# Kernel optimization log

Measured on AMD Instinct MI355X. Metric: run time of the kernel, lower is better.

Reference implementation:

```python
import jax, jax.numpy as jnp
import numpy as np

LEAKY_SLOPE = 0.01  # torch nn.LeakyReLU default


def leaky_relu(x):
    return jnp.where(x >= 0, x, LEAKY_SLOPE * x)


def rgcn_conv(x, edge_index, edge_type, w_rel, w_root, b_conv):
    # PyG RGCNConv: out = x @ W_root + b + sum_r mean_{edges of rel r into i}(x_src @ W_r)
    n = x.shape[0]
    src, dst = edge_index[0], edge_index[1]
    out = x @ w_root + b_conv
    num_rel = w_rel.shape[0]
    for r in range(num_rel):  # small fixed relation count
        mask = (edge_type == r)
        msg = x[src] @ w_rel[r]                      # [E, H]
        msg = jnp.where(mask[:, None], msg, 0.0)
        agg = jax.ops.segment_sum(msg, dst, num_segments=n)          # [N, H]
        cnt = jax.ops.segment_sum(mask.astype(x.dtype), dst, num_segments=n)
        out = out + agg / jnp.maximum(cnt, 1.0)[:, None]             # mean aggr
    return out


def setup_inputs() -> dict:
    key = jax.random.key(0)
    ks = jax.random.split(key, 10)
    N, E, D_IN, H, OUT, R = 50000, 600000, 768, 128, 3, 2
    s_in = 1.0 / np.sqrt(D_IN)
    s_h = 1.0 / np.sqrt(H)
    return {
        "feature": jax.random.normal(ks[0], (N, D_IN), dtype=jnp.float32),
        "edge_index": jax.random.randint(ks[1], (2, E), 0, N, dtype=jnp.int64),
        "edge_type": jax.random.randint(ks[2], (E,), 0, R, dtype=jnp.int64),
        "w_in": jax.random.uniform(ks[3], (D_IN, H), jnp.float32, -s_in, s_in),
        "b_in": jax.random.uniform(ks[4], (H,), jnp.float32, -s_in, s_in),
        "w_rel": jax.random.uniform(ks[5], (R, H, H), jnp.float32, -s_h, s_h),
        "w_root": jax.random.uniform(ks[6], (H, H), jnp.float32, -s_h, s_h),
        "b_conv": jnp.zeros((H,), jnp.float32),
        "w_out": jax.random.uniform(ks[7], (H, OUT), jnp.float32, -s_h, s_h),
        "b_out": jax.random.uniform(ks[8], (OUT,), jnp.float32, -s_h, s_h),
    }


def reference(feature, edge_index, edge_type, w_in, b_in, w_rel, w_root, b_conv, w_out, b_out):
    x = leaky_relu(feature @ w_in + b_in)
    # NOTE: original forward applies rgcn1 twice (shared weights); dropout is
    # identity at inference; rgcn2/linear_relu_output1 are unused.
    x = rgcn_conv(x, edge_index, edge_type, w_rel, w_root, b_conv)
    x = rgcn_conv(x, edge_index, edge_type, w_rel, w_root, b_conv)
    return x @ w_out + b_out
```

## Files before the change

### kernel.cpp

```cpp
#include <hip/hip_runtime.h>

#define H 128
#define CAP 64

typedef _Float16 f16x8 __attribute__((ext_vector_type(8)));
typedef float    f32x4 __attribute__((ext_vector_type(4)));

__global__ __launch_bounds__(256) void hist_fill(const int* __restrict__ src,
    const int* __restrict__ dst, const int* __restrict__ et,
    int* __restrict__ cnt, int* __restrict__ elist, int E, int N)
{
    int e = blockIdx.x * 256 + threadIdx.x;
    if (e >= E) return;
    int s = src[e], d = dst[e], t = et[e];
    int b = t * N + d;
    int pos = atomicAdd(&cnt[b], 1);
    if (pos < CAP) elist[(size_t)b * CAP + pos] = s;
}

__global__ __launch_bounds__(256) void prep_w(const float* __restrict__ w_in,
    const float* __restrict__ w_root, const float* __restrict__ w_rel,
    _Float16* __restrict__ wInT, _Float16* __restrict__ w3T, int K)
{
    int idx = blockIdx.x * 256 + threadIdx.x;
    int tot1 = K * H;
    if (idx < tot1) {
        int k = idx >> 7, c = idx & 127;
        int o = ((k >> 3) << 10) + (c << 3) + (k & 7);
        wInT[o] = (_Float16)w_in[idx];
    } else {
        int i2 = idx - tot1;
        if (i2 < 3 * H * H) {
            int m = i2 / (H * H), r2 = i2 - m * (H * H);
            int c = r2 >> 7, k = r2 & 127;
            const float* s = (m == 0) ? w_root : (w_rel + (size_t)(m - 1) * H * H);
            w3T[i2] = (_Float16)s[(size_t)k * H + c];
        }
    }
}

__device__ __forceinline__ f16x8 cvt8(float4 v0, float4 v1) {
    f16x8 t;
    t[0] = (_Float16)v0.x; t[1] = (_Float16)v0.y; t[2] = (_Float16)v0.z; t[3] = (_Float16)v0.w;
    t[4] = (_Float16)v1.x; t[5] = (_Float16)v1.y; t[6] = (_Float16)v1.z; t[7] = (_Float16)v1.w;
    return t;
}

__global__ __launch_bounds__(256, 2) void gemm_big(const float* __restrict__ A,
    const _Float16* __restrict__ WP, const float* __restrict__ bias,
    _Float16* __restrict__ C16, int M, int K)
{
    const int tid = threadIdx.x;
    const int w   = tid >> 6;
    const int l   = tid & 63;
    const int l15 = l & 15;
    const int q   = l >> 4;
    const int brow = blockIdx.x * 128 + w * 32;

    int r0 = brow + l15;      if (r0 >= M) r0 = M - 1;
    int r1 = brow + 16 + l15; if (r1 >= M) r1 = M - 1;
    const float* ap0 = A + (size_t)r0 * K + q * 8;
    const float* ap1 = A + (size_t)r1 * K + q * 8;
    const _Float16* bp = WP + ((size_t)q * H + l15) * 8;

    float bj[8];
#pragma unroll
    for (int j = 0; j < 8; j++) bj[j] = bias[j * 16 + l15];

    f32x4 acc[2][8];
    const f32x4 z4 = {0.f, 0.f, 0.f, 0.f};
#pragma unroll
    for (int i = 0; i < 2; i++)
#pragma unroll
        for (int j = 0; j < 8; j++) acc[i][j] = z4;

    float4 a00 = *(const float4*)(ap0);
    float4 a01 = *(const float4*)(ap0 + 4);
    float4 a10 = *(const float4*)(ap1);
    float4 a11 = *(const float4*)(ap1 + 4);
    f16x8 bf[8];
#pragma unroll
    for (int j = 0; j < 8; j++) bf[j] = *(const f16x8*)(bp + j * 128);

    const int steps = K / 32;
#pragma unroll 2
    for (int s = 0; s < steps; s++) {
        const bool more = (s + 1) < steps;
        float4 na00, na01, na10, na11; f16x8 nbf[8];
        if (more) {
            const int k0 = (s + 1) * 32;
            na00 = *(const float4*)(ap0 + k0);
            na01 = *(const float4*)(ap0 + k0 + 4);
            na10 = *(const float4*)(ap1 + k0);
            na11 = *(const float4*)(ap1 + k0 + 4);
            const _Float16* nb = bp + (size_t)(s + 1) * 4 * H * 8;
#pragma unroll
            for (int j = 0; j < 8; j++) nbf[j] = *(const f16x8*)(nb + j * 128);
        }
        f16x8 af0 = cvt8(a00, a01);
        f16x8 af1 = cvt8(a10, a11);
#pragma unroll
        for (int j = 0; j < 8; j++) {
            acc[0][j] = __builtin_amdgcn_mfma_f32_16x16x32_f16(af0, bf[j], acc[0][j], 0, 0, 0);
            acc[1][j] = __builtin_amdgcn_mfma_f32_16x16x32_f16(af1, bf[j], acc[1][j], 0, 0, 0);
        }
        if (more) {
            a00 = na00; a01 = na01; a10 = na10; a11 = na11;
#pragma unroll
            for (int j = 0; j < 8; j++) bf[j] = nbf[j];
        }
    }

#pragma unroll
    for (int i = 0; i < 2; i++)
#pragma unroll
        for (int rg = 0; rg < 4; rg++) {
            int row = brow + i * 16 + q * 4 + rg;
            if (row < M) {
#pragma unroll
                for (int j = 0; j < 8; j++) {
                    float v = acc[i][j][rg] + bj[j];
                    v = (v >= 0.f) ? v : 0.01f * v;
                    C16[(size_t)row * H + j * 16 + l15] = (_Float16)v;
                }
            }
        }
}

__global__ __launch_bounds__(512) void gemm3(const _Float16* __restrict__ X16,
    const _Float16* __restrict__ W3, const float* __restrict__ bias,
    float* __restrict__ Y, _Float16* __restrict__ Hh, int M, int mtiles,
    size_t NH)
{
    const int w   = threadIdx.x >> 6;
    const int l   = threadIdx.x & 63;
    const int l15 = l & 15;
    const int q   = l >> 4;
    const int col = w * 16 + l15;

    f16x8 bf[3][4];
#pragma unroll
    for (int m = 0; m < 3; m++) {
        const _Float16* wpp = W3 + (size_t)m * H * H + (size_t)col * H + q * 8;
#pragma unroll
        for (int c = 0; c < 4; c++) bf[m][c] = *(const f16x8*)(wpp + c * 32);
    }
    const float bj = bias[col];

    int t = blockIdx.x;
    if (t >= mtiles) return;
    f16x8 xf[4];
    {
        const _Float16* xp = X16 + ((size_t)t * 16 + l15) * H + q * 8;
#pragma unroll
        for (int c = 0; c < 4; c++) xf[c] = *(const f16x8*)(xp + c * 32);
    }

    const f32x4 z4 = {0.f, 0.f, 0.f, 0.f};
    while (true) {
        int tn = t + gridDim.x;
        bool more = tn < mtiles;
        f16x8 xnf[4];
        if (more) {
            const _Float16* xp = X16 + ((size_t)tn * 16 + l15) * H + q * 8;
#pragma unroll
            for (int c = 0; c < 4; c++) xnf[c] = *(const f16x8*)(xp + c * 32);
        }

        f32x4 a0 = z4, a1 = z4, a2 = z4;
#pragma unroll
        for (int c = 0; c < 4; c++) {
            a0 = __builtin_amdgcn_mfma_f32_16x16x32_f16(xf[c], bf[0][c], a0, 0, 0, 0);
            a1 = __builtin_amdgcn_mfma_f32_16x16x32_f16(xf[c], bf[1][c], a1, 0, 0, 0);
            a2 = __builtin_amdgcn_mfma_f32_16x16x32_f16(xf[c], bf[2][c], a2, 0, 0, 0);
        }

#pragma unroll
        for (int rg = 0; rg < 4; rg++) {
            int row = t * 16 + q * 4 + rg;
            if (row < M) {
                Y [(size_t)row * H + col]      = a0[rg] + bj;
                Hh[(size_t)row * H + col]      = (_Float16)a1[rg];
                Hh[NH + (size_t)row * H + col] = (_Float16)a2[rg];
            }
        }
        if (!more) break;
        t = tn;
#pragma unroll
        for (int c = 0; c < 4; c++) xf[c] = xnf[c];
    }
}

template<int DO_OUT>
__global__ __launch_bounds__(256) void gather_mean(const float* __restrict__ Y,
    const _Float16* __restrict__ h, const int* __restrict__ elist,
    const int* __restrict__ cnt, _Float16* __restrict__ xn, int N, size_t NH,
    const float* __restrict__ Wo, const float* __restrict__ bo,
    float* __restrict__ out)
{
    int wv = blockIdx.x * 4 + (threadIdx.x >> 6);
    int l  = threadIdx.x & 63;
    if (wv >= N) return;

    int d0r = cnt[wv], d1r = cnt[N + wv];
    int d0 = d0r < CAP ? d0r : CAP;
    int d1 = d1r < CAP ? d1r : CAP;
    float inv0 = d0r > 0 ? 1.f / (float)d0r : 0.f;
    float inv1 = d1r > 0 ? 1.f / (float)d1r : 0.f;
    const int* l0 = elist + (size_t)wv * CAP;
    const int* l1 = elist + ((size_t)N + wv) * CAP;
    const int tot = d0 + d1;

    const int eo = l >> 4;
    const int c8 = (l & 15) * 8;

    float wo0[8], wo1[8], wo2[8];
    if (DO_OUT) {
#pragma unroll
        for (int j = 0; j < 8; j++) {
            wo0[j] = Wo[(c8 + j) * 3 + 0];
            wo1[j] = Wo[(c8 + j) * 3 + 1];
            wo2[j] = Wo[(c8 + j) * 3 + 2];
        }
    }

    float acc[8];
#pragma unroll
    for (int j = 0; j < 8; j++) acc[j] = 0.f;

    const f16x8 zv = {};
    for (int p = eo; p < tot; p += 16) {
        int p1 = p + 4, p2 = p + 8, p3 = p + 12;
        bool fA = p < d0;
        int   sA  = fA ? l0[p] : l1[p - d0];
        float scA = fA ? inv0 : inv1;
        f16x8 vA  = *(const f16x8*)&h[(fA ? (size_t)0 : NH) + (size_t)sA * H + c8];
        f16x8 vB = zv, vC = zv, vD = zv;
        float scB = 0.f, scC = 0.f, scD = 0.f;
        if (p1 < tot) {
            bool f = p1 < d0;
            int s = f ? l0[p1] : l1[p1 - d0];
            scB = f ? inv0 : inv1;
            vB = *(const f16x8*)&h[(f ? (size_t)0 : NH) + (size_t)s * H + c8];
        }
        if (p2 < tot) {
            bool f = p2 < d0;
            int s = f ? l0[p2] : l1[p2 - d0];
            scC = f ? inv0 : inv1;
            vC = *(const f16x8*)&h[(f ? (size_t)0 : NH) + (size_t)s * H + c8];
        }
        if (p3 < tot) {
            bool f = p3 < d0;
            int s = f ? l0[p3] : l1[p3 - d0];
            scD = f ? inv0 : inv1;
            vD = *(const f16x8*)&h[(f ? (size_t)0 : NH) + (size_t)s * H + c8];
        }
#pragma unroll
        for (int j = 0; j < 8; j++)
            acc[j] += scA * (float)vA[j] + scB * (float)vB[j]
                    + scC * (float)vC[j] + scD * (float)vD[j];
    }

#pragma unroll
    for (int j = 0; j < 8; j++) {
        acc[j] += __shfl_xor(acc[j], 16);
        acc[j] += __shfl_xor(acc[j], 32);
    }

    float4 y0 = *(const float4*)&Y[(size_t)wv * H + c8];
    float4 y1 = *(const float4*)&Y[(size_t)wv * H + c8 + 4];
    float xv[8];
    xv[0] = acc[0] + y0.x; xv[1] = acc[1] + y0.y;
    xv[2] = acc[2] + y0.z; xv[3] = acc[3] + y0.w;
    xv[4] = acc[4] + y1.x; xv[5] = acc[5] + y1.y;
    xv[6] = acc[6] + y1.z; xv[7] = acc[7] + y1.w;

    if (DO_OUT) {
        float p0 = 0.f, p1 = 0.f, p2 = 0.f;
#pragma unroll
        for (int j = 0; j < 8; j++) {
            p0 += xv[j] * wo0[j];
            p1 += xv[j] * wo1[j];
            p2 += xv[j] * wo2[j];
        }
#pragma unroll
        for (int off = 1; off <= 8; off <<= 1) {
            p0 += __shfl_xor(p0, off);
            p1 += __shfl_xor(p1, off);
            p2 += __shfl_xor(p2, off);
        }
        if (l == 0) {
            out[(size_t)wv * 3 + 0] = p0 + bo[0];
            out[(size_t)wv * 3 + 1] = p1 + bo[1];
            out[(size_t)wv * 3 + 2] = p2 + bo[2];
        }
    } else {
        if (eo == 0) {
            f16x8 o;
#pragma unroll
            for (int j = 0; j < 8; j++) o[j] = (_Float16)xv[j];
            *(f16x8*)&xn[(size_t)wv * H + c8] = o;
        }
    }
}

__global__ __launch_bounds__(256) void out_gemm(const _Float16* __restrict__ X16,
    const float* __restrict__ Wo, const float* __restrict__ bo,
    float* __restrict__ out, int N, int OUT)
{
    int row = blockIdx.x * 4 + (threadIdx.x >> 6);
    int lane = threadIdx.x & 63;
    if (row >= N) return;
    float a0 = (float)X16[(size_t)row * H + lane];
    float a1 = (float)X16[(size_t)row * H + 64 + lane];
    for (int c = 0; c < OUT; c++) {
        float p = a0 * Wo[lane * OUT + c] + a1 * Wo[(64 + lane) * OUT + c];
        for (int off = 32; off > 0; off >>= 1) p += __shfl_down(p, off);
        if (lane == 0) out[(size_t)row * OUT + c] = p + bo[c];
    }
}

extern "C" void kernel_launch(void* const* d_in, const int* in_sizes, int n_in,
                              void* d_out, int out_size, void* d_ws, size_t ws_size,
                              hipStream_t stream) {
    const float* feature = (const float*)d_in[0];
    const int*   ei      = (const int*)d_in[1];
    const int*   et      = (const int*)d_in[2];
    const float* w_in    = (const float*)d_in[3];
    const float* b_in    = (const float*)d_in[4];
    const float* w_rel   = (const float*)d_in[5];
    const float* w_root  = (const float*)d_in[6];
    const float* b_conv  = (const float*)d_in[7];
    const float* w_out   = (const float*)d_in[8];
    const float* b_out   = (const float*)d_in[9];

    const int HH   = in_sizes[4];
    const int D_IN = in_sizes[3] / HH;
    const int N    = in_sizes[0] / D_IN;
    const int E    = in_sizes[1] / 2;
    const int R    = in_sizes[5] / (HH * HH);
    const int OUT  = in_sizes[9];

    const size_t NH = (size_t)N * H;

    char* base = (char*)d_ws;
    _Float16* wInT = (_Float16*)base;
    _Float16* w3T  = wInT + (size_t)D_IN * HH;
    _Float16* x0   = w3T + (size_t)3 * HH * HH;
    _Float16* x1   = x0 + NH;
    _Float16* h    = x1 + NH;
    float* y       = (float*)(h + (size_t)R * NH);
    int* cnt       = (int*)(y + NH);
    int* elist     = cnt + (size_t)R * N;

    hipMemsetAsync(cnt, 0, sizeof(int) * (size_t)R * N, stream);
    prep_w<<<(D_IN * HH + 3 * HH * HH + 255) / 256, 256, 0, stream>>>(
        w_in, w_root, w_rel, wInT, w3T, D_IN);
    hist_fill<<<(E + 255) / 256, 256, 0, stream>>>(ei, ei + E, et, cnt, elist, E, N);

    gemm_big<<<(N + 127) / 128, 256, 0, stream>>>(feature, wInT, b_in, x0, N, D_IN);

    const int mtiles = (N + 15) / 16;
    const int gblocks = (N + 3) / 4;

    gemm3<<<1024, 512, 0, stream>>>(x0, w3T, b_conv, y, h, N, mtiles, NH);
    gather_mean<0><<<gblocks, 256, 0, stream>>>(y, h, elist, cnt, x1, N, NH,
                                                nullptr, nullptr, nullptr);
    gemm3<<<1024, 512, 0, stream>>>(x1, w3T, b_conv, y, h, N, mtiles, NH);
    if (OUT == 3) {
        gather_mean<1><<<gblocks, 256, 0, stream>>>(y, h, elist, cnt, x0, N, NH,
                                                    w_out, b_out, (float*)d_out);
    } else {
        gather_mean<0><<<gblocks, 256, 0, stream>>>(y, h, elist, cnt, x0, N, NH,
                                                    nullptr, nullptr, nullptr);
        out_gemm<<<gblocks, 256, 0, stream>>>(x0, w_out, b_out, (float*)d_out, N, OUT);
    }
}
```

Measured before the change: 450.9 us.

## Shrink gemm_big to 16 rows per wave with ping-pong register prefetch

Each wave in the input GEMM now computes one 16-row tile instead of two, so the grid doubles to 64 rows per block and occupancy is raised to 3 blocks per CU. The k-loop becomes an explicit two-stage ping-pong that loads the next A/B fragments while MFMAs consume the current ones. The intent is to cut register pressure and improve latency hiding for this memory-bound fp32 read of the feature matrix. The cost is that the fp16 weight fragments are reloaded for every 16 rows, doubling B traffic per output row, and the unrolled loop assumes an even number of k-steps, which holds for K=768.

```diff
diff --git a/kernel.cpp b/kernel.cpp
--- a/kernel.cpp
+++ b/kernel.cpp
@@ -46,7 +46,7 @@
     return t;
 }
 
-__global__ __launch_bounds__(256, 2) void gemm_big(const float* __restrict__ A,
+__global__ __launch_bounds__(256, 3) void gemm_big(const float* __restrict__ A,
     const _Float16* __restrict__ WP, const float* __restrict__ bias,
     _Float16* __restrict__ C16, int M, int K)
 {
@@ -55,76 +55,73 @@
     const int l   = tid & 63;
     const int l15 = l & 15;
     const int q   = l >> 4;
-    const int brow = blockIdx.x * 128 + w * 32;
-
-    int r0 = brow + l15;      if (r0 >= M) r0 = M - 1;
-    int r1 = brow + 16 + l15; if (r1 >= M) r1 = M - 1;
-    const float* ap0 = A + (size_t)r0 * K + q * 8;
-    const float* ap1 = A + (size_t)r1 * K + q * 8;
+    const int wrow = blockIdx.x * 64 + w * 16;
+
+    int r0 = wrow + l15; if (r0 >= M) r0 = M - 1;
+    const float* ap = A + (size_t)r0 * K + q * 8;
     const _Float16* bp = WP + ((size_t)q * H + l15) * 8;
 
     float bj[8];
 #pragma unroll
     for (int j = 0; j < 8; j++) bj[j] = bias[j * 16 + l15];
 
-    f32x4 acc[2][8];
+    f32x4 acc[8];
     const f32x4 z4 = {0.f, 0.f, 0.f, 0.f};
 #pragma unroll
-    for (int i = 0; i < 2; i++)
-#pragma unroll
-        for (int j = 0; j < 8; j++) acc[i][j] = z4;
-
-    float4 a00 = *(const float4*)(ap0);
-    float4 a01 = *(const float4*)(ap0 + 4);
-    float4 a10 = *(const float4*)(ap1);
-    float4 a11 = *(const float4*)(ap1 + 4);
-    f16x8 bf[8];
-#pragma unroll
-    for (int j = 0; j < 8; j++) bf[j] = *(const f16x8*)(bp + j * 128);
+    for (int j = 0; j < 8; j++) acc[j] = z4;
+
+    float4 aA0, aA1; f16x8 bA[8];
+    float4 aB0, aB1; f16x8 bB[8];
+
+    aA0 = *(const float4*)(ap);
+    aA1 = *(const float4*)(ap + 4);
+#pragma unroll
+    for (int j = 0; j < 8; j++) bA[j] = *(const f16x8*)(bp + j * 128);
 
     const int steps = K / 32;
-#pragma unroll 2
-    for (int s = 0; s < steps; s++) {
-        const bool more = (s + 1) < steps;
-        float4 na00, na01, na10, na11; f16x8 nbf[8];
-        if (more) {
-            const int k0 = (s + 1) * 32;
-            na00 = *(const float4*)(ap0 + k0);
-            na01 = *(const float4*)(ap0 + k0 + 4);
-            na10 = *(const float4*)(ap1 + k0);
-            na11 = *(const float4*)(ap1 + k0 + 4);
-            const _Float16* nb = bp + (size_t)(s + 1) * 4 * H * 8;
-#pragma unroll
-            for (int j = 0; j < 8; j++) nbf[j] = *(const f16x8*)(nb + j * 128);
-        }
-        f16x8 af0 = cvt8(a00, a01);
-        f16x8 af1 = cvt8(a10, a11);
-#pragma unroll
-        for (int j = 0; j < 8; j++) {
-            acc[0][j] = __builtin_amdgcn_mfma_f32_16x16x32_f16(af0, bf[j], acc[0][j], 0, 0, 0);
-            acc[1][j] = __builtin_amdgcn_mfma_f32_16x16x32_f16(af1, bf[j], acc[1][j], 0, 0, 0);
-        }
-        if (more) {
-            a00 = na00; a01 = na01; a10 = na10; a11 = na11;
-#pragma unroll
-            for (int j = 0; j < 8; j++) bf[j] = nbf[j];
-        }
-    }
-
-#pragma unroll
-    for (int i = 0; i < 2; i++)
-#pragma unroll
-        for (int rg = 0; rg < 4; rg++) {
-            int row = brow + i * 16 + q * 4 + rg;
-            if (row < M) {
-#pragma unroll
-                for (int j = 0; j < 8; j++) {
-                    float v = acc[i][j][rg] + bj[j];
-                    v = (v >= 0.f) ? v : 0.01f * v;
-                    C16[(size_t)row * H + j * 16 + l15] = (_Float16)v;
-                }
+    for (int s = 0; s < steps; s += 2) {
+        {
+            const int k1 = (s + 1) * 32;
+            aB0 = *(const float4*)(ap + k1);
+            aB1 = *(const float4*)(ap + k1 + 4);
+            const _Float16* nb = bp + (size_t)(s + 1) * 4096;
+#pragma unroll
+            for (int j = 0; j < 8; j++) bB[j] = *(const f16x8*)(nb + j * 128);
+        }
+        {
+            f16x8 af = cvt8(aA0, aA1);
+#pragma unroll
+            for (int j = 0; j < 8; j++)
+                acc[j] = __builtin_amdgcn_mfma_f32_16x16x32_f16(af, bA[j], acc[j], 0, 0, 0);
+        }
+        if (s + 2 < steps) {
+            const int k2 = (s + 2) * 32;
+            aA0 = *(const float4*)(ap + k2);
+            aA1 = *(const float4*)(ap + k2 + 4);
+            const _Float16* nb = bp + (size_t)(s + 2) * 4096;
+#pragma unroll
+            for (int j = 0; j < 8; j++) bA[j] = *(const f16x8*)(nb + j * 128);
+        }
+        {
+            f16x8 af = cvt8(aB0, aB1);
+#pragma unroll
+            for (int j = 0; j < 8; j++)
+                acc[j] = __builtin_amdgcn_mfma_f32_16x16x32_f16(af, bB[j], acc[j], 0, 0, 0);
+        }
+    }
+
+#pragma unroll
+    for (int rg = 0; rg < 4; rg++) {
+        int row = wrow + q * 4 + rg;
+        if (row < M) {
+#pragma unroll
+            for (int j = 0; j < 8; j++) {
+                float v = acc[j][rg] + bj[j];
+                v = (v >= 0.f) ? v : 0.01f * v;
+                C16[(size_t)row * H + j * 16 + l15] = (_Float16)v;
             }
         }
+    }
 }
 
 __global__ __launch_bounds__(512) void gemm3(const _Float16* __restrict__ X16,
@@ -358,7 +355,7 @@
         w_in, w_root, w_rel, wInT, w3T, D_IN);
     hist_fill<<<(E + 255) / 256, 256, 0, stream>>>(ei, ei + E, et, cnt, elist, E, N);
 
-    gemm_big<<<(N + 127) / 128, 256, 0, stream>>>(feature, wInT, b_in, x0, N, D_IN);
+    gemm_big<<<(N + 63) / 64, 256, 0, stream>>>(feature, wInT, b_in, x0, N, D_IN);
 
     const int mtiles = (N + 15) / 16;
     const int gblocks = (N + 3) / 4;
```

Measured after the change: 463.3 us. 2.8% more time.
